# Optimization experiments

Measured on AMD Instinct MI355X. Metric: run time of the kernel, lower is better.

The kernel has to match this reference:

```python
import jax, jax.numpy as jnp
import numpy as np

EPS = 1e-10       # module eps
COS_EPS = 1e-8    # torch F.cosine_similarity norm clamp
TAO = 0.0
LIP = 0.0
SQUARED = False
DETACH_HR = True
LAMB_LIP = 1
# p = 1.0 -> np.random.random() < p is always True, so the sampling mask is baked to True.


def setup_inputs() -> dict:
    key = jax.random.key(0)
    k1, k2, k3 = jax.random.split(key, 3)
    img = jax.random.normal(k1, (256, 4, 3, 112, 112), dtype=jnp.float32)
    feat = jax.random.normal(k2, (256, 4, 512), dtype=jnp.float32)
    feat_norm = jax.random.normal(k3, (256, 4, 1), dtype=jnp.float32)
    return {"img": img, "feat": feat, "feat_norm": feat_norm}


def reference(img, feat, feat_norm):
    # img: [B, K, C, H, W], feat: [B, K, D], feat_norm: [B, K, 1]
    fn0 = feat_norm[:, 0, 0]                                   # [B]
    cond = fn0 > -TAO                                          # [B] outer if per batch row
    w = jax.lax.stop_gradient(1.0 / (jnp.exp(fn0) + EPS))      # [B] adaptive weight (detached)

    # consecutive-frame image L2 distance (full-tensor sum per frame pair)
    img_diff = jnp.sqrt(jnp.sum((img[:, 1:] - img[:, :-1]) ** 2, axis=(2, 3, 4))) + EPS  # [B, K-1]
    # skip frames identical to frame 0 (torch.equal check)
    neq = jnp.any(img[:, 1:] != img[:, 0:1], axis=(2, 3, 4))   # [B, K-1]

    fa = feat[:, :-1]                                          # [B, K-1, D] (HR side of each pair)
    fb = feat[:, 1:]                                           # [B, K-1, D]
    if DETACH_HR:
        fa = jax.lax.stop_gradient(fa)
    na = jnp.maximum(jnp.linalg.norm(fa, axis=-1), COS_EPS)
    nb = jnp.maximum(jnp.linalg.norm(fb, axis=-1), COS_EPS)
    cos = jnp.sum(fa * fb, axis=-1) / (na * nb)                # [B, K-1]

    ratio = (1.0 - cos) / img_diff - LIP
    term = ratio ** 2 if SQUARED else jnp.maximum(ratio, 0.0)
    term = term * w[:, None]

    mask = cond[:, None] & neq
    penalty = jnp.sum(jnp.where(mask, term, 0.0), axis=1)      # [B]
    adaptive_weight_list = jnp.where(cond, w, 0.0)             # [B]
    return LAMB_LIP * jnp.mean(penalty), adaptive_weight_list
```

## Files before the change

### kernel.cpp

```cpp
#include <hip/hip_runtime.h>
#include <math.h>

#define EPS 1e-10f
#define COS_EPS 1e-8f

#define NB 256
#define NF 4
#define FRAME_F4 9408
#define BLK_PER_B 37


__global__ void init_ws(float* ws) {
    int i = blockIdx.x * 256 + threadIdx.x;
    if (i < 1536) ws[i] = 0.0f;
}

__global__ __launch_bounds__(256) void img_reduce(const float* __restrict__ img,
                                                  float* __restrict__ ws_sq,
                                                  int* __restrict__ ws_neq) {
    const int b   = blockIdx.y;
    const int tid = threadIdx.x;
    const int idx = blockIdx.x * 256 + tid;

    float s1 = 0.f, s2 = 0.f, s3 = 0.f;
    int   n1 = 0,   n2 = 0,   n3 = 0;

    if (idx < FRAME_F4) {
        const float4* base = (const float4*)img + (size_t)b * NF * FRAME_F4;
        float4 f0 = base[idx];
        float4 f1 = base[FRAME_F4 + idx];
        float4 f2 = base[2 * FRAME_F4 + idx];
        float4 f3 = base[3 * FRAME_F4 + idx];

        float dx, dy, dz, dw;
        dx = f1.x - f0.x; dy = f1.y - f0.y; dz = f1.z - f0.z; dw = f1.w - f0.w;
        s1 = dx*dx + dy*dy + dz*dz + dw*dw;
        dx = f2.x - f1.x; dy = f2.y - f1.y; dz = f2.z - f1.z; dw = f2.w - f1.w;
        s2 = dx*dx + dy*dy + dz*dz + dw*dw;
        dx = f3.x - f2.x; dy = f3.y - f2.y; dz = f3.z - f2.z; dw = f3.w - f2.w;
        s3 = dx*dx + dy*dy + dz*dz + dw*dw;

        n1 = (f1.x != f0.x) | (f1.y != f0.y) | (f1.z != f0.z) | (f1.w != f0.w);
        n2 = (f2.x != f0.x) | (f2.y != f0.y) | (f2.z != f0.z) | (f2.w != f0.w);
        n3 = (f3.x != f0.x) | (f3.y != f0.y) | (f3.z != f0.z) | (f3.w != f0.w);
    }

    for (int off = 32; off > 0; off >>= 1) {
        s1 += __shfl_down(s1, off);
        s2 += __shfl_down(s2, off);
        s3 += __shfl_down(s3, off);
        n1 |= __shfl_down(n1, off);
        n2 |= __shfl_down(n2, off);
        n3 |= __shfl_down(n3, off);
    }

    __shared__ float ls[3][4];
    __shared__ int   ln[3][4];
    const int wave = tid >> 6;
    if ((tid & 63) == 0) {
        ls[0][wave] = s1; ls[1][wave] = s2; ls[2][wave] = s3;
        ln[0][wave] = n1; ln[1][wave] = n2; ln[2][wave] = n3;
    }
    __syncthreads();
    if (tid == 0) {
        float t1 = ls[0][0] + ls[0][1] + ls[0][2] + ls[0][3];
        float t2 = ls[1][0] + ls[1][1] + ls[1][2] + ls[1][3];
        float t3 = ls[2][0] + ls[2][1] + ls[2][2] + ls[2][3];
        int   m1 = ln[0][0] | ln[0][1] | ln[0][2] | ln[0][3];
        int   m2 = ln[1][0] | ln[1][1] | ln[1][2] | ln[1][3];
        int   m3 = ln[2][0] | ln[2][1] | ln[2][2] | ln[2][3];
        atomicAdd(&ws_sq[b * 3 + 0], t1);
        atomicAdd(&ws_sq[b * 3 + 1], t2);
        atomicAdd(&ws_sq[b * 3 + 2], t3);
        if (m1) atomicOr(&ws_neq[b * 3 + 0], 1);
        if (m2) atomicOr(&ws_neq[b * 3 + 1], 1);
        if (m3) atomicOr(&ws_neq[b * 3 + 2], 1);
    }
}

__global__ __launch_bounds__(256) void cos_kernel(const float* __restrict__ feat,
                                                  const float* __restrict__ feat_norm,
                                                  const float* __restrict__ ws_sq,
                                                  const int* __restrict__ ws_neq,
                                                  float* __restrict__ ws_term) {
    const int wid  = blockIdx.x * 4 + (threadIdx.x >> 6);
    const int lane = threadIdx.x & 63;
    const int b = wid / 3;
    const int p = wid % 3;

    const float4* fa = (const float4*)feat + ((size_t)b * NF + p) * 128;
    const float4* fb = fa + 128;

    float dab = 0.f, daa = 0.f, dbb = 0.f;
#pragma unroll
    for (int j = 0; j < 2; ++j) {
        float4 a  = fa[lane + 64 * j];
        float4 bb = fb[lane + 64 * j];
        dab += a.x * bb.x + a.y * bb.y + a.z * bb.z + a.w * bb.w;
        daa += a.x * a.x + a.y * a.y + a.z * a.z + a.w * a.w;
        dbb += bb.x * bb.x + bb.y * bb.y + bb.z * bb.z + bb.w * bb.w;
    }
    for (int off = 32; off > 0; off >>= 1) {
        dab += __shfl_down(dab, off);
        daa += __shfl_down(daa, off);
        dbb += __shfl_down(dbb, off);
    }

    if (lane == 0) {
        float na   = fmaxf(sqrtf(daa), COS_EPS);
        float nb   = fmaxf(sqrtf(dbb), COS_EPS);
        float cosv = dab / (na * nb);
        float img_diff = sqrtf(ws_sq[wid]) + EPS;
        float ratio = (1.0f - cosv) / img_diff;
        float term  = fmaxf(ratio, 0.0f);
        float fn0   = feat_norm[b * NF];
        float w     = 1.0f / (expf(fn0) + EPS);
        bool  cond  = fn0 > 0.0f;
        ws_term[wid] = (cond && ws_neq[wid]) ? term * w : 0.0f;
    }
}

__global__ __launch_bounds__(256) void finalize(const float* __restrict__ feat_norm,
                                                const float* __restrict__ ws_term,
                                                float* __restrict__ out) {
    const int b = threadIdx.x;
    float fn0 = feat_norm[b * NF];
    float w   = 1.0f / (expf(fn0) + EPS);
    bool cond = fn0 > 0.0f;
    out[1 + b] = cond ? w : 0.0f;

    float pen = ws_term[b * 3] + ws_term[b * 3 + 1] + ws_term[b * 3 + 2];
    for (int off = 32; off > 0; off >>= 1) pen += __shfl_down(pen, off);

    __shared__ float sh[4];
    if ((threadIdx.x & 63) == 0) sh[threadIdx.x >> 6] = pen;
    __syncthreads();
    if (threadIdx.x == 0)
        out[0] = (sh[0] + sh[1] + sh[2] + sh[3]) * (1.0f / 256.0f);
}

extern "C" void kernel_launch(void* const* d_in, const int* in_sizes, int n_in,
                              void* d_out, int out_size, void* d_ws, size_t ws_size,
                              hipStream_t stream) {
    const float* img       = (const float*)d_in[0];
    const float* feat      = (const float*)d_in[1];
    const float* feat_norm = (const float*)d_in[2];
    float* out = (float*)d_out;

    float* ws      = (float*)d_ws;
    float* ws_sq   = ws;
    int*   ws_neq  = (int*)(ws + 768);
    float* ws_term = ws + 1536;

    init_ws<<<6, 256, 0, stream>>>(ws);
    img_reduce<<<dim3(BLK_PER_B, NB), 256, 0, stream>>>(img, ws_sq, ws_neq);
    cos_kernel<<<192, 256, 0, stream>>>(feat, feat_norm, ws_sq, ws_neq, ws_term);
    finalize<<<1, 256, 0, stream>>>(feat_norm, ws_term, out);
}
```

Before: 231.0 us.

## Replace atomics with per-block partials and fuse cosine and finalize stages

The image reduction now writes per-block partial sums and not-equal flags into a strided workspace instead of using global atomics, which also removes the init kernel. The cosine and finalize kernels are merged into one per-batch kernel that reduces those partials, computes the terms, writes the weights, and atomically adds to the mean. A memset on the output replaces the workspace zeroing. This drops from four launches to one memset plus two kernels and removes atomic contention in the image stage. In exchange the final mean is accumulated with float atomics, so the summation order is no longer deterministic.

Measured after the change: 223.6 us. 3.2% less time.

```diff
diff --git a/kernel.cpp b/kernel.cpp
--- a/kernel.cpp
+++ b/kernel.cpp
@@ -8,19 +8,16 @@
 #define NF 4
 #define FRAME_F4 9408
 #define BLK_PER_B 37
+#define PART_STRIDE 64
 
 
-__global__ void init_ws(float* ws) {
-    int i = blockIdx.x * 256 + threadIdx.x;
-    if (i < 1536) ws[i] = 0.0f;
-}
-
-__global__ __launch_bounds__(256) void img_reduce(const float* __restrict__ img,
-                                                  float* __restrict__ ws_sq,
-                                                  int* __restrict__ ws_neq) {
+__global__ __launch_bounds__(256) void img_stage(const float* __restrict__ img,
+                                                 float* __restrict__ ws_sq_part,
+                                                 int* __restrict__ ws_neq_part) {
     const int b   = blockIdx.y;
+    const int bx  = blockIdx.x;
     const int tid = threadIdx.x;
-    const int idx = blockIdx.x * 256 + tid;
+    const int idx = bx * 256 + tid;
 
     float s1 = 0.f, s2 = 0.f, s3 = 0.f;
     int   n1 = 0,   n2 = 0,   n3 = 0;
@@ -63,30 +60,25 @@
     }
     __syncthreads();
     if (tid == 0) {
-        float t1 = ls[0][0] + ls[0][1] + ls[0][2] + ls[0][3];
-        float t2 = ls[1][0] + ls[1][1] + ls[1][2] + ls[1][3];
-        float t3 = ls[2][0] + ls[2][1] + ls[2][2] + ls[2][3];
-        int   m1 = ln[0][0] | ln[0][1] | ln[0][2] | ln[0][3];
-        int   m2 = ln[1][0] | ln[1][1] | ln[1][2] | ln[1][3];
-        int   m3 = ln[2][0] | ln[2][1] | ln[2][2] | ln[2][3];
-        atomicAdd(&ws_sq[b * 3 + 0], t1);
-        atomicAdd(&ws_sq[b * 3 + 1], t2);
-        atomicAdd(&ws_sq[b * 3 + 2], t3);
-        if (m1) atomicOr(&ws_neq[b * 3 + 0], 1);
-        if (m2) atomicOr(&ws_neq[b * 3 + 1], 1);
-        if (m3) atomicOr(&ws_neq[b * 3 + 2], 1);
+        const int base3 = b * 3;
+        ws_sq_part[(base3 + 0) * PART_STRIDE + bx] = ls[0][0] + ls[0][1] + ls[0][2] + ls[0][3];
+        ws_sq_part[(base3 + 1) * PART_STRIDE + bx] = ls[1][0] + ls[1][1] + ls[1][2] + ls[1][3];
+        ws_sq_part[(base3 + 2) * PART_STRIDE + bx] = ls[2][0] + ls[2][1] + ls[2][2] + ls[2][3];
+        ws_neq_part[(base3 + 0) * PART_STRIDE + bx] = ln[0][0] | ln[0][1] | ln[0][2] | ln[0][3];
+        ws_neq_part[(base3 + 1) * PART_STRIDE + bx] = ln[1][0] | ln[1][1] | ln[1][2] | ln[1][3];
+        ws_neq_part[(base3 + 2) * PART_STRIDE + bx] = ln[2][0] | ln[2][1] | ln[2][2] | ln[2][3];
     }
 }
 
-__global__ __launch_bounds__(256) void cos_kernel(const float* __restrict__ feat,
-                                                  const float* __restrict__ feat_norm,
-                                                  const float* __restrict__ ws_sq,
-                                                  const int* __restrict__ ws_neq,
-                                                  float* __restrict__ ws_term) {
-    const int wid  = blockIdx.x * 4 + (threadIdx.x >> 6);
-    const int lane = threadIdx.x & 63;
-    const int b = wid / 3;
-    const int p = wid % 3;
+__global__ __launch_bounds__(192) void batch_stage(const float* __restrict__ feat,
+                                                   const float* __restrict__ feat_norm,
+                                                   const float* __restrict__ ws_sq_part,
+                                                   const int* __restrict__ ws_neq_part,
+                                                   float* __restrict__ out) {
+    const int b    = blockIdx.x;
+    const int tid  = threadIdx.x;
+    const int p    = tid >> 6;
+    const int lane = tid & 63;
 
     const float4* fa = (const float4*)feat + ((size_t)b * NF + p) * 128;
     const float4* fb = fa + 128;
@@ -100,43 +92,40 @@
         daa += a.x * a.x + a.y * a.y + a.z * a.z + a.w * a.w;
         dbb += bb.x * bb.x + bb.y * bb.y + bb.z * bb.z + bb.w * bb.w;
     }
+
+    const int slot = (b * 3 + p) * PART_STRIDE + lane;
+    float sq = (lane < BLK_PER_B) ? ws_sq_part[slot] : 0.0f;
+    int   nq = (lane < BLK_PER_B) ? ws_neq_part[slot] : 0;
+
     for (int off = 32; off > 0; off >>= 1) {
         dab += __shfl_down(dab, off);
         daa += __shfl_down(daa, off);
         dbb += __shfl_down(dbb, off);
+        sq  += __shfl_down(sq, off);
+        nq  |= __shfl_down(nq, off);
     }
 
+    __shared__ float sh_term[3];
     if (lane == 0) {
         float na   = fmaxf(sqrtf(daa), COS_EPS);
         float nb   = fmaxf(sqrtf(dbb), COS_EPS);
         float cosv = dab / (na * nb);
-        float img_diff = sqrtf(ws_sq[wid]) + EPS;
+        float img_diff = sqrtf(sq) + EPS;
         float ratio = (1.0f - cosv) / img_diff;
         float term  = fmaxf(ratio, 0.0f);
         float fn0   = feat_norm[b * NF];
         float w     = 1.0f / (expf(fn0) + EPS);
         bool  cond  = fn0 > 0.0f;
-        ws_term[wid] = (cond && ws_neq[wid]) ? term * w : 0.0f;
+        sh_term[p]  = (cond && nq) ? term * w : 0.0f;
     }
-}
-
-__global__ __launch_bounds__(256) void finalize(const float* __restrict__ feat_norm,
-                                                const float* __restrict__ ws_term,
-                                                float* __restrict__ out) {
-    const int b = threadIdx.x;
-    float fn0 = feat_norm[b * NF];
-    float w   = 1.0f / (expf(fn0) + EPS);
-    bool cond = fn0 > 0.0f;
-    out[1 + b] = cond ? w : 0.0f;
-
-    float pen = ws_term[b * 3] + ws_term[b * 3 + 1] + ws_term[b * 3 + 2];
-    for (int off = 32; off > 0; off >>= 1) pen += __shfl_down(pen, off);
-
-    __shared__ float sh[4];
-    if ((threadIdx.x & 63) == 0) sh[threadIdx.x >> 6] = pen;
     __syncthreads();
-    if (threadIdx.x == 0)
-        out[0] = (sh[0] + sh[1] + sh[2] + sh[3]) * (1.0f / 256.0f);
+    if (tid == 0) {
+        float fn0 = feat_norm[b * NF];
+        float w   = 1.0f / (expf(fn0) + EPS);
+        out[1 + b] = (fn0 > 0.0f) ? w : 0.0f;
+        float pen = sh_term[0] + sh_term[1] + sh_term[2];
+        atomicAdd(&out[0], pen * (1.0f / 256.0f));
+    }
 }
 
 extern "C" void kernel_launch(void* const* d_in, const int* in_sizes, int n_in,
@@ -147,13 +136,10 @@
     const float* feat_norm = (const float*)d_in[2];
     float* out = (float*)d_out;
 
-    float* ws      = (float*)d_ws;
-    float* ws_sq   = ws;
-    int*   ws_neq  = (int*)(ws + 768);
-    float* ws_term = ws + 1536;
+    float* ws_sq_part = (float*)d_ws;
+    int*   ws_neq_part = (int*)((char*)d_ws + 768 * PART_STRIDE * sizeof(float));
 
-    init_ws<<<6, 256, 0, stream>>>(ws);
-    img_reduce<<<dim3(BLK_PER_B, NB), 256, 0, stream>>>(img, ws_sq, ws_neq);
-    cos_kernel<<<192, 256, 0, stream>>>(feat, feat_norm, ws_sq, ws_neq, ws_term);
-    finalize<<<1, 256, 0, stream>>>(feat_norm, ws_term, out);
+    hipMemsetAsync(out, 0, sizeof(float), stream);
+    img_stage<<<dim3(BLK_PER_B, NB), 256, 0, stream>>>(img, ws_sq_part, ws_neq_part);
+    batch_stage<<<NB, 192, 0, stream>>>(feat, feat_norm, ws_sq_part, ws_neq_part, out);
 }
```
